# Kernel optimization log

Hardware: AMD Instinct MI355X
Metric: run time of the kernel (lower is better)

The kernel has to match this reference:

```python
import jax, jax.numpy as jnp
import numpy as np

B, T, D, N_ITER, SR = 32, 1024, 1024, 256, 4


def setup_inputs() -> dict:
    key = jax.random.key(0)
    k1, k2 = jax.random.split(key)
    xs = jax.random.normal(k1, (B, T, D), dtype=jnp.float32)
    ds = jax.random.uniform(k2, (B, T, N_ITER), dtype=jnp.float32)
    return {"xs": xs, "ds": ds, "is_inference": 1}


def _linear_interp(d, f):
    # d: (B, T) velocity field sampled on the integer grid; f: (B, T) fractional positions
    Tn = d.shape[-1]
    i0 = jnp.clip(jnp.floor(f).astype(jnp.int32), 0, Tn - 2)
    t = f - i0.astype(f.dtype)
    d0 = jnp.take_along_axis(d, i0, axis=-1)
    d1 = jnp.take_along_axis(d, i0 + 1, axis=-1)
    return d0 + t * (d1 - d0)


def _gw_ode(ds):
    # ds: (B, T, N) per-step warp increments (already divided by N*sr).
    # m=1 init: f = identity grid + first field; then N-1 Euler steps f += d_i(f).
    Bb, Tn, N = ds.shape
    grid = jnp.arange(Tn, dtype=ds.dtype)[None, :]
    f0 = jnp.clip(grid + ds[:, :, 0], 0.0, Tn - 1.0)

    def step(f, d):
        f = jnp.clip(f + _linear_interp(d, f), 0.0, Tn - 1.0)
        return f, None

    d_steps = jnp.moveaxis(ds[:, :, 1:], -1, 0)  # (N-1, B, T)
    f, _ = jax.lax.scan(step, f0, d_steps)
    return f


def _cubic_interpolation(x, f):
    # Catmull-Rom cubic resampling. x: (B, D, T) channel-first; f: (B, T) positions.
    Tn = x.shape[-1]
    i1 = jnp.clip(jnp.floor(f).astype(jnp.int32), 0, Tn - 1)
    t = (f - i1.astype(f.dtype))[:, None, :]  # (B, 1, T)

    def gat(idx):
        idx = jnp.clip(idx, 0, Tn - 1)
        return jnp.take_along_axis(x, jnp.broadcast_to(idx[:, None, :], x.shape), axis=-1)

    p0, p1, p2, p3 = gat(i1 - 1), gat(i1), gat(i1 + 1), gat(i1 + 2)
    t2 = t * t
    t3 = t2 * t
    w0 = -0.5 * t3 + t2 - 0.5 * t
    w1 = 1.5 * t3 - 2.5 * t2 + 1.0
    w2 = -1.5 * t3 + 2.0 * t2 + 0.5 * t
    w3 = 0.5 * t3 - 0.5 * t2
    return w0 * p0 + w1 * p1 + w2 * p2 + w3 * p3


def reference(xs, ds, is_inference):
    ds = ds / (ds.shape[-1] * SR)
    f = _gw_ode(ds)                                   # (B, T) warp function
    ys = _cubic_interpolation(jnp.swapaxes(xs, -1, -2), f)  # (B, D, T)
    return jnp.swapaxes(ys, -1, -2), f
```

## Files before the change

### kernel.cpp

```cpp
#include <hip/hip_runtime.h>

#define BB 32
#define TT 1024
#define DD 1024
#define NIT 256
#define SRR 4
#define KT 8

typedef float vf4 __attribute__((ext_vector_type(4)));

__global__ __launch_bounds__(256, 4) void fused2_kernel(const float* __restrict__ xs,
                                                        const float* __restrict__ ds,
                                                        float* __restrict__ out_ys,
                                                        float* __restrict__ f_out) {
    __shared__ float fbuf[KT];

    const int nwg = BB * (TT / KT);
    const int blk = (blockIdx.x & 7) * (nwg >> 3) + (blockIdx.x >> 3);
    const int b   = blk >> 7;
    const int t0  = (blk & 127) * KT;
    const int tid = threadIdx.x;
    const float inv = 1.0f / (float)(NIT * SRR);

    {
        const int k = tid >> 5;
        const int j = tid & 31;
        const int t = t0 + k;
        const int r0 = (t < TT - 2) ? t : (TT - 2);

        const float4* row0 = (const float4*)ds + (size_t)(b * TT + r0) * (NIT / 4) + j * 2;
        const float4* row1 = row0 + (NIT / 4);
        float d0v[8], d1v[8];
#pragma unroll
        for (int m = 0; m < 2; ++m) {
            const float4 u = row0[m];
            d0v[4*m+0] = u.x; d0v[4*m+1] = u.y; d0v[4*m+2] = u.z; d0v[4*m+3] = u.w;
            const float4 v = row1[m];
            d1v[4*m+0] = v.x; d1v[4*m+1] = v.y; d1v[4*m+2] = v.z; d1v[4*m+3] = v.w;
        }

        float g0 = 0.0f;
        if (j == 0) {
            const float dinit = (t == r0) ? d0v[0] : d1v[0];
            float f0 = (float)t + dinit * inv;
            f0 = fminf(fmaxf(f0, 0.0f), (float)(TT - 1));
            g0 = f0 - (float)r0;
        }
        g0 = __shfl(g0, 0, 32);

        float A = 1.0f, Bc = 0.0f;
#pragma unroll
        for (int m = 0; m < 8; ++m) {
            float a  = fmaf(d1v[m] - d0v[m], inv, 1.0f);
            float bb = d0v[m] * inv;
            if (m == 0) { if (j == 0) { a = 1.0f; bb = 0.0f; } }
            Bc = fmaf(Bc, a, bb);
            A  = A * a;
        }

#pragma unroll
        for (int d = 1; d < 32; d <<= 1) {
            const float Ap = __shfl_up(A, d, 32);
            const float Bp = __shfl_up(Bc, d, 32);
            if (j >= d) {
                Bc = fmaf(Bp, A, Bc);
                A  = A * Ap;
            }
        }

        const float Ae = __shfl_up(A, 1, 32);
        const float Be = __shfl_up(Bc, 1, 32);
        float g = (j == 0) ? g0 : fmaf(g0, Ae, Be);

        const float lo = -(float)r0;
        const float hi = (float)(TT - 1 - r0);
        const bool edge = (r0 == TT - 2);
        bool bad = false;
#pragma unroll
        for (int m = 0; m < 8; ++m) {
            float a  = fmaf(d1v[m] - d0v[m], inv, 1.0f);
            float bb = d0v[m] * inv;
            if (m == 0) { if (j == 0) { a = 1.0f; bb = 0.0f; } }
            g = fmaf(g, a, bb);
            g = fminf(fmaxf(g, lo), hi);
            bad |= (g < 0.0f) | ((g >= 1.0f) & !(edge & (g == hi)));
        }

        const unsigned long long bm = __ballot(bad);
        const int lane = tid & 63;
        const bool chainbad = ((bm >> (lane & ~31)) & 0xFFFFFFFFull) != 0;

        if (j == 31) {
            float fres = (float)r0 + g;
            if (chainbad) {
                float f = (float)t + ds[(size_t)(b * TT + t) * NIT] * inv;
                f = fminf(fmaxf(f, 0.0f), (float)(TT - 1));
                for (int i = 1; i < NIT; ++i) {
                    int i0 = (int)floorf(f);
                    i0 = min(max(i0, 0), TT - 2);
                    const float dd0 = ds[(size_t)(b * TT + i0) * NIT + i] * inv;
                    const float dd1 = ds[(size_t)(b * TT + i0 + 1) * NIT + i] * inv;
                    const float tf = f - (float)i0;
                    f = fminf(fmaxf(f + dd0 + tf * (dd1 - dd0), 0.0f), (float)(TT - 1));
                }
                fres = f;
            }
            fbuf[k] = fres;
            f_out[b * TT + t] = fres;
        }
    }
    __syncthreads();

    const float4* X = (const float4*)xs + (size_t)b * TT * (DD / 4);
    vf4* O = (vf4*)out_ys;

    for (int k = 0; k < KT; ++k) {
        const float fv = fbuf[k];
        int i1 = (int)floorf(fv);
        i1 = min(max(i1, 0), TT - 1);
        const float tf = fv - (float)i1;
        const float t2 = tf * tf, t3 = t2 * tf;
        const float w0 = -0.5f * t3 + t2 - 0.5f * tf;
        const float w1 = 1.5f * t3 - 2.5f * t2 + 1.0f;
        const float w2 = -1.5f * t3 + 2.0f * t2 + 0.5f * tf;
        const float w3 = 0.5f * t3 - 0.5f * t2;

        const int j0 = max(i1 - 1, 0);
        const int j2 = min(i1 + 1, TT - 1);
        const int j3 = min(i1 + 2, TT - 1);

        const float4 p0 = X[((size_t)j0 << 8) + tid];
        const float4 p1 = X[((size_t)i1 << 8) + tid];
        const float4 p2 = X[((size_t)j2 << 8) + tid];
        const float4 p3 = X[((size_t)j3 << 8) + tid];
        vf4 v;
        v.x = w0 * p0.x + w1 * p1.x + w2 * p2.x + w3 * p3.x;
        v.y = w0 * p0.y + w1 * p1.y + w2 * p2.y + w3 * p3.y;
        v.z = w0 * p0.z + w1 * p1.z + w2 * p2.z + w3 * p3.z;
        v.w = w0 * p0.w + w1 * p1.w + w2 * p2.w + w3 * p3.w;
        __builtin_nontemporal_store(v, O + (((size_t)(b * TT + t0 + k)) << 8) + tid);
    }
}

extern "C" void kernel_launch(void* const* d_in, const int* in_sizes, int n_in,
                              void* d_out, int out_size, void* d_ws, size_t ws_size,
                              hipStream_t stream) {
    const float* xs = (const float*)d_in[0];
    const float* ds = (const float*)d_in[1];

    float* out_ys = (float*)d_out;
    float* out_f  = out_ys + (size_t)BB * TT * DD;

    fused2_kernel<<<dim3(BB * (TT / KT)), 256, 0, stream>>>(xs, ds, out_ys, out_f);
}
```

Before: 49.65 us.

## Prefetch xs row window before ODE scan and reuse it across cubic taps

Loads the 11 xs rows covering t0-1..t0+9 into registers at kernel start, before the warp-ODE scan, so their memory latency overlaps the ODE computation. The unrolled cubic stage reuses these registers when the warped index equals the output index, otherwise falls back to gathering from global memory. This removes redundant per-tap loads and serialized load latency after the barrier, at the cost of extra register pressure and wasted loads when the warp shifts rows.

```diff
diff --git a/kernel.cpp b/kernel.cpp
--- a/kernel.cpp
+++ b/kernel.cpp
@@ -9,7 +9,7 @@
 
 typedef float vf4 __attribute__((ext_vector_type(4)));
 
-__global__ __launch_bounds__(256, 4) void fused2_kernel(const float* __restrict__ xs,
+__global__ __launch_bounds__(256, 4) void fused3_kernel(const float* __restrict__ xs,
                                                         const float* __restrict__ ds,
                                                         float* __restrict__ out_ys,
                                                         float* __restrict__ f_out) {
@@ -21,6 +21,13 @@
     const int t0  = (blk & 127) * KT;
     const int tid = threadIdx.x;
     const float inv = 1.0f / (float)(NIT * SRR);
+
+    const float4* X = (const float4*)xs + (size_t)b * TT * (DD / 4);
+#define WROW(r) X[((size_t)min(max(t0 - 1 + (r), 0), TT - 1) << 8) + tid]
+    const float4 wA = WROW(0), wB = WROW(1), wC = WROW(2), wD = WROW(3);
+    const float4 wE = WROW(4), wF = WROW(5), wG = WROW(6), wH = WROW(7);
+    const float4 wI = WROW(8), wJ = WROW(9), wK = WROW(10);
+#undef WROW
 
     {
         const int k = tid >> 5;
@@ -111,35 +118,49 @@
     }
     __syncthreads();
 
-    const float4* X = (const float4*)xs + (size_t)b * TT * (DD / 4);
     vf4* O = (vf4*)out_ys;
 
-    for (int k = 0; k < KT; ++k) {
-        const float fv = fbuf[k];
-        int i1 = (int)floorf(fv);
-        i1 = min(max(i1, 0), TT - 1);
-        const float tf = fv - (float)i1;
-        const float t2 = tf * tf, t3 = t2 * tf;
-        const float w0 = -0.5f * t3 + t2 - 0.5f * tf;
-        const float w1 = 1.5f * t3 - 2.5f * t2 + 1.0f;
-        const float w2 = -1.5f * t3 + 2.0f * t2 + 0.5f * tf;
-        const float w3 = 0.5f * t3 - 0.5f * t2;
+#define CUBIC_K(k, q0, q1, q2, q3)                                                   \
+    {                                                                                \
+        const int t = t0 + (k);                                                      \
+        const float fv = fbuf[(k)];                                                  \
+        int i1 = (int)floorf(fv);                                                    \
+        i1 = min(max(i1, 0), TT - 1);                                                \
+        const float tf = fv - (float)i1;                                             \
+        const float t2 = tf * tf, t3 = t2 * tf;                                      \
+        const float c0 = -0.5f * t3 + t2 - 0.5f * tf;                                \
+        const float c1 = 1.5f * t3 - 2.5f * t2 + 1.0f;                               \
+        const float c2 = -1.5f * t3 + 2.0f * t2 + 0.5f * tf;                         \
+        const float c3 = 0.5f * t3 - 0.5f * t2;                                      \
+        float4 p0, p1, p2, p3;                                                       \
+        if (i1 == t) {                                  \
+            p0 = (q0); p1 = (q1); p2 = (q2); p3 = (q3);                              \
+        } else {                                 \
+            const int j0 = max(i1 - 1, 0);                                           \
+            const int j2 = min(i1 + 1, TT - 1);                                      \
+            const int j3 = min(i1 + 2, TT - 1);                                      \
+            p0 = X[((size_t)j0 << 8) + tid];                                         \
+            p1 = X[((size_t)i1 << 8) + tid];                                         \
+            p2 = X[((size_t)j2 << 8) + tid];                                         \
+            p3 = X[((size_t)j3 << 8) + tid];                                         \
+        }                                                                            \
+        vf4 v;                                                                       \
+        v.x = c0 * p0.x + c1 * p1.x + c2 * p2.x + c3 * p3.x;                         \
+        v.y = c0 * p0.y + c1 * p1.y + c2 * p2.y + c3 * p3.y;                         \
+        v.z = c0 * p0.z + c1 * p1.z + c2 * p2.z + c3 * p3.z;                         \
+        v.w = c0 * p0.w + c1 * p1.w + c2 * p2.w + c3 * p3.w;                         \
+        __builtin_nontemporal_store(v, O + (((size_t)(b * TT + t)) << 8) + tid);     \
+    }
 
-        const int j0 = max(i1 - 1, 0);
-        const int j2 = min(i1 + 1, TT - 1);
-        const int j3 = min(i1 + 2, TT - 1);
-
-        const float4 p0 = X[((size_t)j0 << 8) + tid];
-        const float4 p1 = X[((size_t)i1 << 8) + tid];
-        const float4 p2 = X[((size_t)j2 << 8) + tid];
-        const float4 p3 = X[((size_t)j3 << 8) + tid];
-        vf4 v;
-        v.x = w0 * p0.x + w1 * p1.x + w2 * p2.x + w3 * p3.x;
-        v.y = w0 * p0.y + w1 * p1.y + w2 * p2.y + w3 * p3.y;
-        v.z = w0 * p0.z + w1 * p1.z + w2 * p2.z + w3 * p3.z;
-        v.w = w0 * p0.w + w1 * p1.w + w2 * p2.w + w3 * p3.w;
-        __builtin_nontemporal_store(v, O + (((size_t)(b * TT + t0 + k)) << 8) + tid);
-    }
+    CUBIC_K(0, wA, wB, wC, wD)
+    CUBIC_K(1, wB, wC, wD, wE)
+    CUBIC_K(2, wC, wD, wE, wF)
+    CUBIC_K(3, wD, wE, wF, wG)
+    CUBIC_K(4, wE, wF, wG, wH)
+    CUBIC_K(5, wF, wG, wH, wI)
+    CUBIC_K(6, wG, wH, wI, wJ)
+    CUBIC_K(7, wH, wI, wJ, wK)
+#undef CUBIC_K
 }
 
 extern "C" void kernel_launch(void* const* d_in, const int* in_sizes, int n_in,
@@ -151,5 +172,5 @@
     float* out_ys = (float*)d_out;
     float* out_f  = out_ys + (size_t)BB * TT * DD;
 
-    fused2_kernel<<<dim3(BB * (TT / KT)), 256, 0, stream>>>(xs, ds, out_ys, out_f);
+    fused3_kernel<<<dim3(BB * (TT / KT)), 256, 0, stream>>>(xs, ds, out_ys, out_f);
 }
```

New measurement: 48.82 us. Within noise of the previous version (-1.7%).
